# Kernel optimization log

Hardware: AMD Instinct MI355X
Metric: run time of the kernel (lower is better)

The kernel has to match this reference:

```python
import jax, jax.numpy as jnp
import numpy as np

D_MODEL = 512
N_HEADS = 8
D_K = D_MODEL // N_HEADS


def setup_inputs() -> dict:
    key = jax.random.key(0)
    ks = jax.random.split(key, 12)
    B, L = 2, 512
    s = 1.0 / np.sqrt(D_MODEL)
    sk = 1.0 / np.sqrt(D_K)
    return {
        "query": jax.random.normal(ks[0], (B, L, D_MODEL), jnp.float32),
        "key": jax.random.normal(ks[1], (B, L, D_MODEL), jnp.float32),
        "value": jax.random.normal(ks[2], (B, L, D_MODEL), jnp.float32),
        "Wq": jax.random.normal(ks[3], (D_MODEL, D_MODEL), jnp.float32) * s,
        "bq": jnp.zeros((D_MODEL,), jnp.float32),
        "Wk": jax.random.normal(ks[4], (D_MODEL, D_MODEL), jnp.float32) * s,
        "bk": jnp.zeros((D_MODEL,), jnp.float32),
        "Wv": jax.random.normal(ks[5], (D_MODEL, D_MODEL), jnp.float32) * s,
        "bv": jnp.zeros((D_MODEL,), jnp.float32),
        "Wo": jax.random.normal(ks[6], (D_MODEL, D_MODEL), jnp.float32) * s,
        "bo": jnp.zeros((D_MODEL,), jnp.float32),
        "Aq": jax.random.normal(ks[7], (D_K, D_K), jnp.float32) * sk,  # inner W_q (no bias)
        "Ak": jax.random.normal(ks[8], (D_K, D_K), jnp.float32) * sk,  # inner W_k (no bias)
        "av": jax.random.normal(ks[9], (D_K,), jnp.float32) * sk,      # inner v (d_k -> 1)
    }


def _split_heads(x):
    B, L, _ = x.shape
    return x.reshape(B, L, N_HEADS, D_K).transpose(0, 2, 1, 3)  # [B,H,L,dk]


def reference(query, key, value, Wq, bq, Wk, bk, Wv, bv, Wo, bo, Aq, Ak, av):
    # outer projections (torch Linear: x @ W.T + b)
    Q = _split_heads(query @ Wq.T + bq)   # [B,H,Lq,dk]
    K = _split_heads(key @ Wk.T + bk)     # [B,H,Lk,dk]
    V = _split_heads(value @ Wv.T + bv)   # [B,H,Lk,dk]
    # inner additive attention: e_ij = v^T tanh(Aq q_i + Ak k_j)
    qp = Q @ Aq.T                          # [B,H,Lq,dk]
    kp = K @ Ak.T                          # [B,H,Lk,dk]
    energy = jnp.tanh(qp[:, :, :, None, :] + kp[:, :, None, :, :])  # [B,H,Lq,Lk,dk]
    scores = jnp.einsum('bhqkd,d->bhqk', energy, av)
    attn = jax.nn.softmax(scores, axis=-1)  # dropout disabled (eval)
    out = jnp.einsum('bhqk,bhkd->bhqd', attn, V)  # [B,H,Lq,dk]
    B, _, Lq, _ = out.shape
    out = out.transpose(0, 2, 1, 3).reshape(B, Lq, D_MODEL)
    return out @ Wo.T + bo
```

## Files before the change

### kernel.cpp

```cpp
#include <hip/hip_runtime.h>

#define LOG2E 1.4426950408889634f

typedef __bf16 bf16x8 __attribute__((ext_vector_type(8)));
typedef float f32x4 __attribute__((ext_vector_type(4)));
typedef float f32x2 __attribute__((ext_vector_type(2)));
typedef unsigned short u16x8 __attribute__((ext_vector_type(8)));

__device__ __forceinline__ unsigned short bfb(__bf16 b){
  union { __bf16 b; unsigned short u; } z; z.b = b; return z.u;
}


__global__ __launch_bounds__(256) void prep_all(
    const float* __restrict__ Wq, const float* __restrict__ Aq,
    const float* __restrict__ Wk, const float* __restrict__ Ak,
    const float* __restrict__ bq, const float* __restrict__ bk,
    const float* __restrict__ av,
    const float* __restrict__ Wv, const float* __restrict__ Wo,
    const float* __restrict__ Qin, const float* __restrict__ Kin,
    const float* __restrict__ Vin,
    unsigned short* __restrict__ W2qp, unsigned short* __restrict__ W2kp,
    unsigned short* __restrict__ Wvp,  unsigned short* __restrict__ Wop,
    unsigned short* __restrict__ qhi, unsigned short* __restrict__ qlo,
    unsigned short* __restrict__ khi, unsigned short* __restrict__ klo,
    unsigned short* __restrict__ vhi, unsigned short* __restrict__ vlo,
    float* __restrict__ b2q, float* __restrict__ b2k, float* __restrict__ av2g,
    float* __restrict__ zbase){
  if (blockIdx.x >= 513){
    if (blockIdx.y){
      int x = blockIdx.x - 513;
      if (x < 260){
        float* z = zbase + (size_t)(x * 256 + threadIdx.x) * 8;
        f32x4 zz = {0.f, 0.f, 0.f, 0.f};
        *(f32x4*)z = zz;
        *(f32x4*)(z + 4) = zz;
      }
      return;
    }
    int j = blockIdx.x - 513;
    const float* src; unsigned short *dh, *dl;
    if (j < 256){ src = Qin; dh = qhi; dl = qlo; }
    else if (j < 512){ src = Kin; dh = khi; dl = klo; j -= 256; }
    else { src = Vin; dh = vhi; dl = vlo; j -= 512; }
    int base = (j * 256 + threadIdx.x) * 8;
    f32x4 v0 = *(const f32x4*)(src + base);
    f32x4 v1 = *(const f32x4*)(src + base + 4);
    u16x8 hh, ll;
    #pragma unroll
    for (int t = 0; t < 8; t++){
      float f = (t < 4) ? v0[t] : v1[t - 4];
      __bf16 hb = (__bf16)f;
      hh[t] = bfb(hb);
      ll[t] = bfb((__bf16)(f - (float)hb));
    }
    *(u16x8*)(dh + base) = hh;
    *(u16x8*)(dl + base) = ll;
    return;
  }
  if (blockIdx.x >= 256){
    if (blockIdx.x == 512){
      if (blockIdx.y == 0){
        #pragma unroll
        for (int rep = 0; rep < 2; rep++){
          int n = rep * 256 + threadIdx.x;
          int h = n >> 6, e = n & 63;
          float aq = 0.f, ak = 0.f;
          for (int c = 0; c < 64; c++){
            aq += Aq[e*64 + c] * bq[h*64 + c];
            ak += Ak[e*64 + c] * bk[h*64 + c];
          }
          b2q[n] = aq * (2.f * LOG2E);
          b2k[n] = ak * (2.f * LOG2E);
        }
      } else {
        if (threadIdx.x < 64) av2g[threadIdx.x] = -2.f * LOG2E * av[threadIdx.x];
      }
      return;
    }
    const float* src = blockIdx.y ? Wo : Wv;
    unsigned short* dst = blockIdx.y ? Wop : Wvp;
    int base = ((blockIdx.x - 256) * 256 + threadIdx.x) * 4;
    int n = base >> 9, k0 = base & 511;
    float4 v = *(const float4*)(src + base);
    ushort4 h, l;
    float f; __bf16 hb;
    f = v.x; hb = (__bf16)f; h.x = bfb(hb); l.x = bfb((__bf16)(f - (float)hb));
    f = v.y; hb = (__bf16)f; h.y = bfb(hb); l.y = bfb((__bf16)(f - (float)hb));
    f = v.z; hb = (__bf16)f; h.z = bfb(hb); l.z = bfb((__bf16)(f - (float)hb));
    f = v.w; hb = (__bf16)f; h.w = bfb(hb); l.w = bfb((__bf16)(f - (float)hb));
    int nt = n >> 4, ln = n & 15;
    int ks = k0 >> 5, q = (k0 & 31) >> 3, j0 = k0 & 7;
    size_t off = (size_t)((nt*16 + ks) * 2) * 512 + (q*16 + ln) * 8 + j0;
    *(ushort4*)(dst + off)       = h;
    *(ushort4*)(dst + off + 512) = l;
    return;
  }
  const float* W  = blockIdx.y ? Wk : Wq;
  const float* Am = blockIdx.y ? Ak : Aq;
  unsigned short* dst = blockIdx.y ? W2kp : W2qp;
  int idx = blockIdx.x * 256 + threadIdx.x;
  int n = idx >> 7;
  int k0 = (idx & 127) * 4;
  int h = n >> 6, e = n & 63;
  float4 acc = {0.f, 0.f, 0.f, 0.f};
  #pragma unroll 8
  for (int c = 0; c < 64; c++){
    float am = Am[e*64 + c];
    float4 wv = *(const float4*)(W + (size_t)(h*64 + c)*512 + k0);
    acc.x += am * wv.x;
    acc.y += am * wv.y;
    acc.z += am * wv.z;
    acc.w += am * wv.w;
  }
  int nt = n >> 4, ln = n & 15;
  int ks = k0 >> 5, q = (k0 & 31) >> 3, j0 = k0 & 7;
  size_t off = (size_t)((nt*16 + ks) * 2) * 512 + (q*16 + ln) * 8 + j0;
  ushort4 hh, ll;
  float f; __bf16 hb;
  f = acc.x * (2.f * LOG2E); hb = (__bf16)f; hh.x = bfb(hb); ll.x = bfb((__bf16)(f - (float)hb));
  f = acc.y * (2.f * LOG2E); hb = (__bf16)f; hh.y = bfb(hb); ll.y = bfb((__bf16)(f - (float)hb));
  f = acc.z * (2.f * LOG2E); hb = (__bf16)f; hh.z = bfb(hb); ll.z = bfb((__bf16)(f - (float)hb));
  f = acc.w * (2.f * LOG2E); hb = (__bf16)f; hh.w = bfb(hb); ll.w = bfb((__bf16)(f - (float)hb));
  *(ushort4*)(dst + off)       = hh;
  *(ushort4*)(dst + off + 512) = ll;
}

struct GemmBatch {
  const unsigned short* Ahi;
  const unsigned short* Alo;
  const unsigned short* Bp;
  const float* bias;
  float* Cf;
  unsigned short* Chi;
  unsigned short* Clo;
  int transposed;
  int expout;
  int dual;
};
struct GemmArgs { GemmBatch g[3]; };

__global__ __launch_bounds__(256) void gemm_nk(GemmArgs ga){
  GemmBatch gb = ga.g[blockIdx.z];
  __shared__ unsigned short AhiS[32 * 72];
  __shared__ unsigned short AloS[32 * 72];
  const int tid = threadIdx.x, lane = tid & 63, w = tid >> 6;
  const int l15 = lane & 15, quad = lane >> 4;
  const int m0  = blockIdx.x * 32;
  const int nt0 = blockIdx.y * 4;
  const int wr = w >> 1, wc = w & 1;
  f32x4 ac0 = {0.f,0.f,0.f,0.f}, ac1 = ac0;

  const int srow = tid >> 3;
  const int scol = (tid & 7) * 8;
  const unsigned short* srcH = gb.Ahi + (size_t)(m0 + srow) * 512 + scol;
  const unsigned short* srcL = gb.Alo + (size_t)(m0 + srow) * 512 + scol;
  unsigned short* dstH = &AhiS[srow * 72 + scol];
  unsigned short* dstL = &AloS[srow * 72 + scol];
  u16x8 ph = *(const u16x8*)srcH;
  u16x8 pl = *(const u16x8*)srcL;

  const int arow = (wr * 16 + l15) * 72;

  for (int kc = 0; kc < 8; kc++){
    __syncthreads();
    *(u16x8*)dstH = ph;
    *(u16x8*)dstL = pl;
    if (kc < 7){
      ph = *(const u16x8*)(srcH + (kc + 1) * 64);
      pl = *(const u16x8*)(srcL + (kc + 1) * 64);
    }
    __syncthreads();
    #pragma unroll
    for (int s = 0; s < 2; s++){
      int ks = kc * 2 + s;
      bf16x8 ah = *(const bf16x8*)&AhiS[arow + s*32 + quad*8];
      bf16x8 al = *(const bf16x8*)&AloS[arow + s*32 + quad*8];
      #pragma unroll
      for (int t = 0; t < 2; t++){
        int nt = nt0 + wc*2 + t;
        const unsigned short* bp = gb.Bp + (size_t)((nt*16 + ks) * 2) * 512 + lane*8;
        bf16x8 bh = *(const bf16x8*)bp;
        bf16x8 bl = *(const bf16x8*)(bp + 512);
        f32x4& ac = t ? ac1 : ac0;
        ac = __builtin_amdgcn_mfma_f32_16x16x32_bf16(ah, bh, ac, 0, 0, 0);
        ac = __builtin_amdgcn_mfma_f32_16x16x32_bf16(al, bh, ac, 0, 0, 0);
        ac = __builtin_amdgcn_mfma_f32_16x16x32_bf16(ah, bl, ac, 0, 0, 0);
      }
    }
  }

  const int mrow = m0 + wr * 16 + quad * 4;
  #pragma unroll
  for (int t = 0; t < 2; t++){
    f32x4 v = t ? ac1 : ac0;
    int n = nt0*16 + wc*32 + t*16 + l15;
    float bs = gb.bias[n];
    #pragma unroll
    for (int r = 0; r < 4; r++){
      float val = v[r] + bs;
      if (gb.expout) val = __builtin_amdgcn_exp2f(val);
      int m2 = mrow + r;
      if (gb.dual){
        size_t o = (size_t)(((m2 >> 9) * 8 + (n >> 6)) * 64 + (n & 63)) * 512 + (m2 & 511);
        __bf16 hb = (__bf16)val;
        gb.Chi[o] = bfb(hb);
        gb.Clo[o] = bfb((__bf16)(val - (float)hb));
      } else if (gb.transposed){
        gb.Cf[(size_t)(((m2 >> 9) * 8 + (n >> 6)) * 512 + (m2 & 511)) * 64 + (n & 63)] = val;
      } else {
        gb.Cf[(size_t)m2 * 512 + n] = val;
      }
    }
  }
}

__global__ __launch_bounds__(256, 3) void score_pv(
    const float* __restrict__ eqQ, const float* __restrict__ ekp,
    const float* __restrict__ av2g,
    const unsigned short* __restrict__ vthi, const unsigned short* __restrict__ vtlo,
    float* __restrict__ Og, float* __restrict__ deng){
  __shared__ float SHf[12480];
  float* EKt = SHf;
  float* EQs = SHf + 8320;
  float* avS = SHf + 12416;
  unsigned short* Ph = (unsigned short*)SHf;
  unsigned short* Pl = (unsigned short*)SHf + 8704;

  const int tid = threadIdx.x, lane = tid & 63, w = tid >> 6;
  const int l15 = lane & 15, quad = lane >> 4;
  const int bh = blockIdx.z, b = bh >> 3, h = bh & 7;
  const int i0 = blockIdx.y * 64;
  const int j0 = blockIdx.x * 128;

  {
    int r = tid >> 2, c = (tid & 3) * 16;
    const float* s = eqQ + ((size_t)bh * 512 + i0 + r) * 64 + c;
    #pragma unroll
    for (int u = 0; u < 4; u++)
      *(f32x4*)&EQs[r * 64 + c + u * 4] = *(const f32x4*)(s + u * 4);
  }
  if (tid < 64) avS[tid] = av2g[tid];
  {
    int j = tid >> 1, c0 = (tid & 1) * 32;
    const float* s = ekp + ((size_t)(b * 512) + j0 + j) * 512 + h * 64 + c0;
    #pragma unroll
    for (int u = 0; u < 8; u++){
      f32x4 v = *(const f32x4*)(s + u * 4);
      #pragma unroll
      for (int q = 0; q < 4; q++) EKt[(c0 + u * 4 + q) * 130 + j] = v[q];
    }
  }
  __syncthreads();

  f32x2 acc[16];
  #pragma unroll
  for (int ii = 0; ii < 16; ii++) acc[ii] = (f32x2){0.f, 0.f};
  for (int d = 0; d < 64; d += 4){
    f32x2 ek0 = *(const f32x2*)&EKt[(d    ) * 130 + 2 * lane];
    f32x2 ek1 = *(const f32x2*)&EKt[(d + 1) * 130 + 2 * lane];
    f32x2 ek2 = *(const f32x2*)&EKt[(d + 2) * 130 + 2 * lane];
    f32x2 ek3 = *(const f32x2*)&EKt[(d + 3) * 130 + 2 * lane];
    f32x4 a4 = *(const f32x4*)&avS[d];
    #pragma unroll
    for (int ii = 0; ii < 16; ii++){
      f32x4 eq4 = *(const f32x4*)&EQs[(w * 16 + ii) * 64 + d];
      f32x2 A = __builtin_elementwise_fma((f32x2){eq4[0], eq4[0]}, ek0, (f32x2){1.f, 1.f});
      f32x2 B = __builtin_elementwise_fma((f32x2){eq4[1], eq4[1]}, ek1, (f32x2){1.f, 1.f});
      f32x2 t = __builtin_elementwise_fma((f32x2){a4[1], a4[1]}, A, (f32x2){a4[0], a4[0]} * B);
      f32x2 dpr = A * B;
      f32x2 r;
      r.x = __builtin_amdgcn_rcpf(dpr.x);
      r.y = __builtin_amdgcn_rcpf(dpr.y);
      acc[ii] = __builtin_elementwise_fma(t, r, acc[ii]);
      f32x2 C = __builtin_elementwise_fma((f32x2){eq4[2], eq4[2]}, ek2, (f32x2){1.f, 1.f});
      f32x2 D = __builtin_elementwise_fma((f32x2){eq4[3], eq4[3]}, ek3, (f32x2){1.f, 1.f});
      f32x2 t2 = __builtin_elementwise_fma((f32x2){a4[3], a4[3]}, C, (f32x2){a4[2], a4[2]} * D);
      f32x2 dpr2 = C * D;
      f32x2 r2;
      r2.x = __builtin_amdgcn_rcpf(dpr2.x);
      r2.y = __builtin_amdgcn_rcpf(dpr2.y);
      acc[ii] = __builtin_elementwise_fma(t2, r2, acc[ii]);
    }
  }
  #pragma unroll
  for (int ii = 0; ii < 16; ii++){
    acc[ii].x = __builtin_amdgcn_exp2f(acc[ii].x);
    acc[ii].y = __builtin_amdgcn_exp2f(acc[ii].y);
  }
  __syncthreads();
  #pragma unroll
  for (int ii = 0; ii < 16; ii++){
    float s2 = acc[ii].x + acc[ii].y;
    #pragma unroll
    for (int off = 1; off < 64; off <<= 1) s2 += __shfl_xor(s2, off, 64);
    if (lane == 0) atomicAdd(&deng[bh * 512 + i0 + w * 16 + ii], s2);
    __bf16 h0 = (__bf16)acc[ii].x, h1 = (__bf16)acc[ii].y;
    ushort2 hi = { bfb(h0), bfb(h1) };
    ushort2 lo = { bfb((__bf16)(acc[ii].x - (float)h0)), bfb((__bf16)(acc[ii].y - (float)h1)) };
    *(ushort2*)&Ph[(w * 16 + ii) * 136 + 2 * lane] = hi;
    *(ushort2*)&Pl[(w * 16 + ii) * 136 + 2 * lane] = lo;
  }
  __syncthreads();

  f32x4 o0 = {0.f,0.f,0.f,0.f}, o1 = o0, o2 = o0, o3 = o0;
  const size_t vbase = ((size_t)bh * 64) * 512 + j0;
  #pragma unroll
  for (int ks = 0; ks < 4; ks++){
    bf16x8 pa = *(const bf16x8*)&Ph[(w * 16 + l15) * 136 + ks * 32 + quad * 8];
    bf16x8 pb = *(const bf16x8*)&Pl[(w * 16 + l15) * 136 + ks * 32 + quad * 8];
    #pragma unroll
    for (int nt = 0; nt < 4; nt++){
      size_t vo = vbase + (size_t)(nt * 16 + l15) * 512 + ks * 32 + quad * 8;
      bf16x8 vh = *(const bf16x8*)(vthi + vo);
      bf16x8 vl = *(const bf16x8*)(vtlo + vo);
      f32x4& o = nt == 0 ? o0 : nt == 1 ? o1 : nt == 2 ? o2 : o3;
      o = __builtin_amdgcn_mfma_f32_16x16x32_bf16(pa, vh, o, 0, 0, 0);
      o = __builtin_amdgcn_mfma_f32_16x16x32_bf16(pb, vh, o, 0, 0, 0);
      o = __builtin_amdgcn_mfma_f32_16x16x32_bf16(pa, vl, o, 0, 0, 0);
    }
  }
  #pragma unroll
  for (int nt = 0; nt < 4; nt++){
    f32x4 o = nt == 0 ? o0 : nt == 1 ? o1 : nt == 2 ? o2 : o3;
    int d = nt * 16 + l15;
    #pragma unroll
    for (int r = 0; r < 4; r++){
      int i = i0 + w * 16 + quad * 4 + r;
      atomicAdd(&Og[((size_t)bh * 512 + i) * 64 + d], o[r]);
    }
  }
}

__global__ __launch_bounds__(256) void finish_oh(
    const float* __restrict__ Og, const float* __restrict__ deng,
    unsigned short* __restrict__ Ohhi, unsigned short* __restrict__ Ohlo){
  int t = blockIdx.x * 256 + threadIdx.x;
  int bh = t >> 12;
  int i  = (t >> 3) & 511;
  int d0 = (t & 7) * 8;
  float rv = 1.0f / deng[bh * 512 + i];
  const float* src = Og + ((size_t)bh * 512 + i) * 64 + d0;
  f32x4 v0 = *(const f32x4*)src;
  f32x4 v1 = *(const f32x4*)(src + 4);
  u16x8 hh, ll;
  #pragma unroll
  for (int u = 0; u < 8; u++){
    float f = ((u < 4) ? v0[u] : v1[u - 4]) * rv;
    __bf16 hb = (__bf16)f;
    hh[u] = bfb(hb);
    ll[u] = bfb((__bf16)(f - (float)hb));
  }
  size_t o = ((size_t)(bh >> 3) * 512 + i) * 512 + (bh & 7) * 64 + d0;
  *(u16x8*)(Ohhi + o) = hh;
  *(u16x8*)(Ohlo + o) = ll;
}

extern "C" void kernel_launch(void* const* d_in, const int* in_sizes, int n_in,
                              void* d_out, int out_size, void* d_ws, size_t ws_size,
                              hipStream_t stream){
  const float* q_in = (const float*)d_in[0];
  const float* k_in = (const float*)d_in[1];
  const float* v_in = (const float*)d_in[2];
  const float* Wq_  = (const float*)d_in[3];
  const float* bq_  = (const float*)d_in[4];
  const float* Wk_  = (const float*)d_in[5];
  const float* bk_  = (const float*)d_in[6];
  const float* Wv_  = (const float*)d_in[7];
  const float* bv_  = (const float*)d_in[8];
  const float* Wo_  = (const float*)d_in[9];
  const float* bo_  = (const float*)d_in[10];
  const float* Aq_  = (const float*)d_in[11];
  const float* Ak_  = (const float*)d_in[12];
  const float* av_  = (const float*)d_in[13];

  char* ws = (char*)d_ws;
  unsigned short* W2qp = (unsigned short*)(ws + 0);
  unsigned short* W2kp = (unsigned short*)(ws + 1048576);
  unsigned short* Ohhi = (unsigned short*)(ws + 0);
  unsigned short* Ohlo = (unsigned short*)(ws + 1048576);
  unsigned short* Wvp  = (unsigned short*)(ws + 2097152);
  unsigned short* Wop  = (unsigned short*)(ws + 3145728);
  float* b2q  = (float*)(ws + 4194304);
  float* b2k  = (float*)(ws + 4196352);
  float* av2g = (float*)(ws + 4198400);
  float* eqQ  = (float*)(ws + 4198656);
  float* ekp  = (float*)(ws + 6295808);
  unsigned short* vthi = (unsigned short*)(ws + 8392960);
  unsigned short* vtlo = (unsigned short*)(ws + 9441536);
  unsigned short* qhi = (unsigned short*)(ws + 10490112);
  unsigned short* qlo = (unsigned short*)(ws + 11538688);
  unsigned short* khi = (unsigned short*)(ws + 12587264);
  unsigned short* klo = (unsigned short*)(ws + 13635840);
  unsigned short* vhi = (unsigned short*)(ws + 14684416);
  unsigned short* vlo = (unsigned short*)(ws + 15732992);
  float* deng = (float*)(ws + 16781568);
  float* Og   = (float*)(ws + 16814336);

  prep_all<<<dim3(1281, 2, 1), 256, 0, stream>>>(Wq_, Aq_, Wk_, Ak_, bq_, bk_, av_,
                                                 Wv_, Wo_, q_in, k_in, v_in,
                                                 W2qp, W2kp, Wvp, Wop,
                                                 qhi, qlo, khi, klo, vhi, vlo,
                                                 b2q, b2k, av2g, deng);

  GemmArgs ga;
  ga.g[0] = { qhi, qlo, W2qp, b2q, eqQ, 0, 0, 1, 1, 0 };
  ga.g[1] = { khi, klo, W2kp, b2k, ekp, 0, 0, 0, 1, 0 };
  ga.g[2] = { vhi, vlo, Wvp,  bv_, 0, vthi, vtlo, 0, 0, 1 };
  gemm_nk<<<dim3(32, 8, 3), 256, 0, stream>>>(ga);

  score_pv<<<dim3(4, 8, 16), 256, 0, stream>>>(eqQ, ekp, av2g, vthi, vtlo, Og, deng);

  finish_oh<<<dim3(256, 1, 1), 256, 0, stream>>>(Og, deng, Ohhi, Ohlo);

  GemmArgs go;
  go.g[0] = { Ohhi, Ohlo, Wop, bo_, (float*)d_out, 0, 0, 0, 0, 0 };
  go.g[1] = go.g[0];
  go.g[2] = go.g[0];
  gemm_nk<<<dim3(32, 8, 1), 256, 0, stream>>>(go);
}
```

Baseline: 163.6 us.

## Split score kernel key range across twice the waves and stage dual GEMM output

The score_pv kernel now runs 512 threads per block. Each wave pair covers the same 16 query rows but a different 64-key half, so each lane handles one key instead of two. The two halves' P·V partial results are summed in shared memory before one set of atomics, which halves the global atomic traffic to the output buffer. In the projection GEMM, the transposed bf16 hi/lo output for V is first staged through shared memory so it can be written with 16-byte coalesced stores instead of scattered 2-byte stores. The cost is a tighter per-thread register budget from the new launch bounds and an extra barrier and LDS round trip.

```diff
diff --git a/kernel.cpp b/kernel.cpp
--- a/kernel.cpp
+++ b/kernel.cpp
@@ -142,8 +142,8 @@
 
 __global__ __launch_bounds__(256) void gemm_nk(GemmArgs ga){
   GemmBatch gb = ga.g[blockIdx.z];
-  __shared__ unsigned short AhiS[32 * 72];
-  __shared__ unsigned short AloS[32 * 72];
+  __shared__ unsigned short AhiS[64 * 40];
+  __shared__ unsigned short AloS[64 * 40];
   const int tid = threadIdx.x, lane = tid & 63, w = tid >> 6;
   const int l15 = lane & 15, quad = lane >> 4;
   const int m0  = blockIdx.x * 32;
@@ -190,6 +190,32 @@
     }
   }
 
+  if (gb.dual){
+    __syncthreads();
+    #pragma unroll
+    for (int t = 0; t < 2; t++){
+      f32x4 v = t ? ac1 : ac0;
+      int nl = wc*32 + t*16 + l15;
+      float bs = gb.bias[nt0*16 + nl];
+      #pragma unroll
+      for (int r = 0; r < 4; r++){
+        float val = v[r] + bs;
+        int ml = wr*16 + quad*4 + r;
+        __bf16 hb = (__bf16)val;
+        AhiS[nl*40 + ml] = bfb(hb);
+        AloS[nl*40 + ml] = bfb((__bf16)(val - (float)hb));
+      }
+    }
+    __syncthreads();
+    int nl = tid >> 2, mq = (tid & 3) * 8;
+    int hh2 = (nt0 * 16) >> 6;
+    int b2 = m0 >> 9;
+    size_t o = (size_t)((b2*8 + hh2)*64 + ((nt0*16 + nl) & 63)) * 512 + (m0 & 511) + mq;
+    *(u16x8*)(gb.Chi + o) = *(const u16x8*)&AhiS[nl*40 + mq];
+    *(u16x8*)(gb.Clo + o) = *(const u16x8*)&AloS[nl*40 + mq];
+    return;
+  }
+
   const int mrow = m0 + wr * 16 + quad * 4;
   #pragma unroll
   for (int t = 0; t < 2; t++){
@@ -201,12 +227,7 @@
       float val = v[r] + bs;
       if (gb.expout) val = __builtin_amdgcn_exp2f(val);
       int m2 = mrow + r;
-      if (gb.dual){
-        size_t o = (size_t)(((m2 >> 9) * 8 + (n >> 6)) * 64 + (n & 63)) * 512 + (m2 & 511);
-        __bf16 hb = (__bf16)val;
-        gb.Chi[o] = bfb(hb);
-        gb.Clo[o] = bfb((__bf16)(val - (float)hb));
-      } else if (gb.transposed){
+      if (gb.transposed){
         gb.Cf[(size_t)(((m2 >> 9) * 8 + (n >> 6)) * 512 + (m2 & 511)) * 64 + (n & 63)] = val;
       } else {
         gb.Cf[(size_t)m2 * 512 + n] = val;
@@ -215,33 +236,27 @@
   }
 }
 
-__global__ __launch_bounds__(256, 3) void score_pv(
+__global__ __launch_bounds__(512, 4) void score_pv(
     const float* __restrict__ eqQ, const float* __restrict__ ekp,
     const float* __restrict__ av2g,
     const unsigned short* __restrict__ vthi, const unsigned short* __restrict__ vtlo,
     float* __restrict__ Og, float* __restrict__ deng){
-  __shared__ float SHf[12480];
+  __shared__ float SHf[12864];
   float* EKt = SHf;
   float* EQs = SHf + 8320;
-  float* avS = SHf + 12416;
+  float* avS = SHf + 12800;
   unsigned short* Ph = (unsigned short*)SHf;
   unsigned short* Pl = (unsigned short*)SHf + 8704;
+  float* cmb = SHf + 8704;
 
   const int tid = threadIdx.x, lane = tid & 63, w = tid >> 6;
   const int l15 = lane & 15, quad = lane >> 4;
   const int bh = blockIdx.z, b = bh >> 3, h = bh & 7;
   const int i0 = blockIdx.y * 64;
   const int j0 = blockIdx.x * 128;
-
-  {
-    int r = tid >> 2, c = (tid & 3) * 16;
-    const float* s = eqQ + ((size_t)bh * 512 + i0 + r) * 64 + c;
-    #pragma unroll
-    for (int u = 0; u < 4; u++)
-      *(f32x4*)&EQs[r * 64 + c + u * 4] = *(const f32x4*)(s + u * 4);
-  }
-  if (tid < 64) avS[tid] = av2g[tid];
-  {
+  const int wi = w >> 1, jh = w & 1;
+
+  if (tid < 256){
     int j = tid >> 1, c0 = (tid & 1) * 32;
     const float* s = ekp + ((size_t)(b * 512) + j0 + j) * 512 + h * 64 + c0;
     #pragma unroll
@@ -250,65 +265,63 @@
       #pragma unroll
       for (int q = 0; q < 4; q++) EKt[(c0 + u * 4 + q) * 130 + j] = v[q];
     }
+  } else {
+    int t2 = tid - 256;
+    int r = t2 >> 2, c = (t2 & 3) * 16;
+    const float* s = eqQ + ((size_t)bh * 512 + i0 + r) * 64 + c;
+    #pragma unroll
+    for (int u = 0; u < 4; u++)
+      *(f32x4*)&EQs[r * 64 + c + u * 4] = *(const f32x4*)(s + u * 4);
+    if (t2 < 64) avS[t2] = av2g[t2];
   }
   __syncthreads();
 
-  f32x2 acc[16];
-  #pragma unroll
-  for (int ii = 0; ii < 16; ii++) acc[ii] = (f32x2){0.f, 0.f};
+  float acc[16];
+  #pragma unroll
+  for (int ii = 0; ii < 16; ii++) acc[ii] = 0.f;
+  const int jl = jh * 64 + lane;
   for (int d = 0; d < 64; d += 4){
-    f32x2 ek0 = *(const f32x2*)&EKt[(d    ) * 130 + 2 * lane];
-    f32x2 ek1 = *(const f32x2*)&EKt[(d + 1) * 130 + 2 * lane];
-    f32x2 ek2 = *(const f32x2*)&EKt[(d + 2) * 130 + 2 * lane];
-    f32x2 ek3 = *(const f32x2*)&EKt[(d + 3) * 130 + 2 * lane];
+    float ek0 = EKt[(d    ) * 130 + jl];
+    float ek1 = EKt[(d + 1) * 130 + jl];
+    float ek2 = EKt[(d + 2) * 130 + jl];
+    float ek3 = EKt[(d + 3) * 130 + jl];
     f32x4 a4 = *(const f32x4*)&avS[d];
     #pragma unroll
     for (int ii = 0; ii < 16; ii++){
-      f32x4 eq4 = *(const f32x4*)&EQs[(w * 16 + ii) * 64 + d];
-      f32x2 A = __builtin_elementwise_fma((f32x2){eq4[0], eq4[0]}, ek0, (f32x2){1.f, 1.f});
-      f32x2 B = __builtin_elementwise_fma((f32x2){eq4[1], eq4[1]}, ek1, (f32x2){1.f, 1.f});
-      f32x2 t = __builtin_elementwise_fma((f32x2){a4[1], a4[1]}, A, (f32x2){a4[0], a4[0]} * B);
-      f32x2 dpr = A * B;
-      f32x2 r;
-      r.x = __builtin_amdgcn_rcpf(dpr.x);
-      r.y = __builtin_amdgcn_rcpf(dpr.y);
-      acc[ii] = __builtin_elementwise_fma(t, r, acc[ii]);
-      f32x2 C = __builtin_elementwise_fma((f32x2){eq4[2], eq4[2]}, ek2, (f32x2){1.f, 1.f});
-      f32x2 D = __builtin_elementwise_fma((f32x2){eq4[3], eq4[3]}, ek3, (f32x2){1.f, 1.f});
-      f32x2 t2 = __builtin_elementwise_fma((f32x2){a4[3], a4[3]}, C, (f32x2){a4[2], a4[2]} * D);
-      f32x2 dpr2 = C * D;
-      f32x2 r2;
-      r2.x = __builtin_amdgcn_rcpf(dpr2.x);
-      r2.y = __builtin_amdgcn_rcpf(dpr2.y);
-      acc[ii] = __builtin_elementwise_fma(t2, r2, acc[ii]);
-    }
-  }
+      f32x4 eq4 = *(const f32x4*)&EQs[(wi * 16 + ii) * 64 + d];
+      float A = __builtin_fmaf(eq4[0], ek0, 1.f);
+      float B = __builtin_fmaf(eq4[1], ek1, 1.f);
+      float t = __builtin_fmaf(a4[1], A, a4[0] * B);
+      acc[ii] = __builtin_fmaf(t, __builtin_amdgcn_rcpf(A * B), acc[ii]);
+      float C = __builtin_fmaf(eq4[2], ek2, 1.f);
+      float D = __builtin_fmaf(eq4[3], ek3, 1.f);
+      float t2 = __builtin_fmaf(a4[3], C, a4[2] * D);
+      acc[ii] = __builtin_fmaf(t2, __builtin_amdgcn_rcpf(C * D), acc[ii]);
+    }
+  }
+  #pragma unroll
+  for (int ii = 0; ii < 16; ii++) acc[ii] = __builtin_amdgcn_exp2f(acc[ii]);
+  __syncthreads();
+
   #pragma unroll
   for (int ii = 0; ii < 16; ii++){
-    acc[ii].x = __builtin_amdgcn_exp2f(acc[ii].x);
-    acc[ii].y = __builtin_amdgcn_exp2f(acc[ii].y);
-  }
-  __syncthreads();
-  #pragma unroll
-  for (int ii = 0; ii < 16; ii++){
-    float s2 = acc[ii].x + acc[ii].y;
+    float s2 = acc[ii];
     #pragma unroll
     for (int off = 1; off < 64; off <<= 1) s2 += __shfl_xor(s2, off, 64);
-    if (lane == 0) atomicAdd(&deng[bh * 512 + i0 + w * 16 + ii], s2);
-    __bf16 h0 = (__bf16)acc[ii].x, h1 = (__bf16)acc[ii].y;
-    ushort2 hi = { bfb(h0), bfb(h1) };
-    ushort2 lo = { bfb((__bf16)(acc[ii].x - (float)h0)), bfb((__bf16)(acc[ii].y - (float)h1)) };
-    *(ushort2*)&Ph[(w * 16 + ii) * 136 + 2 * lane] = hi;
-    *(ushort2*)&Pl[(w * 16 + ii) * 136 + 2 * lane] = lo;
-  }
-  __syncthreads();
+    if (lane == 0) atomicAdd(&deng[bh * 512 + i0 + wi * 16 + ii], s2);
+    float e = acc[ii];
+    __bf16 hb = (__bf16)e;
+    Ph[(wi * 16 + ii) * 136 + jl] = bfb(hb);
+    Pl[(wi * 16 + ii) * 136 + jl] = bfb((__bf16)(e - (float)hb));
+  }
 
   f32x4 o0 = {0.f,0.f,0.f,0.f}, o1 = o0, o2 = o0, o3 = o0;
-  const size_t vbase = ((size_t)bh * 64) * 512 + j0;
-  #pragma unroll
-  for (int ks = 0; ks < 4; ks++){
-    bf16x8 pa = *(const bf16x8*)&Ph[(w * 16 + l15) * 136 + ks * 32 + quad * 8];
-    bf16x8 pb = *(const bf16x8*)&Pl[(w * 16 + l15) * 136 + ks * 32 + quad * 8];
+  const size_t vbase = ((size_t)bh * 64) * 512 + j0 + jh * 64;
+  #pragma unroll
+  for (int ks = 0; ks < 2; ks++){
+    int k0 = jh * 64 + ks * 32 + quad * 8;
+    bf16x8 pa = *(const bf16x8*)&Ph[(wi * 16 + l15) * 136 + k0];
+    bf16x8 pb = *(const bf16x8*)&Pl[(wi * 16 + l15) * 136 + k0];
     #pragma unroll
     for (int nt = 0; nt < 4; nt++){
       size_t vo = vbase + (size_t)(nt * 16 + l15) * 512 + ks * 32 + quad * 8;
@@ -320,14 +333,27 @@
       o = __builtin_amdgcn_mfma_f32_16x16x32_bf16(pa, vl, o, 0, 0, 0);
     }
   }
-  #pragma unroll
-  for (int nt = 0; nt < 4; nt++){
-    f32x4 o = nt == 0 ? o0 : nt == 1 ? o1 : nt == 2 ? o2 : o3;
-    int d = nt * 16 + l15;
-    #pragma unroll
-    for (int r = 0; r < 4; r++){
-      int i = i0 + w * 16 + quad * 4 + r;
-      atomicAdd(&Og[((size_t)bh * 512 + i) * 64 + d], o[r]);
+  if (jh == 1){
+    #pragma unroll
+    for (int nt = 0; nt < 4; nt++){
+      f32x4 o = nt == 0 ? o0 : nt == 1 ? o1 : nt == 2 ? o2 : o3;
+      #pragma unroll
+      for (int r = 0; r < 4; r++)
+        cmb[(wi * 16 + quad * 4 + r) * 64 + nt * 16 + l15] = o[r];
+    }
+  }
+  __syncthreads();
+  if (jh == 0){
+    #pragma unroll
+    for (int nt = 0; nt < 4; nt++){
+      f32x4 o = nt == 0 ? o0 : nt == 1 ? o1 : nt == 2 ? o2 : o3;
+      int d = nt * 16 + l15;
+      #pragma unroll
+      for (int r = 0; r < 4; r++){
+        int il = wi * 16 + quad * 4 + r;
+        float cv = o[r] + cmb[il * 64 + d];
+        atomicAdd(&Og[((size_t)bh * 512 + i0 + il) * 64 + d], cv);
+      }
     }
   }
 }
@@ -409,7 +435,7 @@
   ga.g[2] = { vhi, vlo, Wvp,  bv_, 0, vthi, vtlo, 0, 0, 1 };
   gemm_nk<<<dim3(32, 8, 3), 256, 0, stream>>>(ga);
 
-  score_pv<<<dim3(4, 8, 16), 256, 0, stream>>>(eqQ, ekp, av2g, vthi, vtlo, Og, deng);
+  score_pv<<<dim3(4, 8, 16), 512, 0, stream>>>(eqQ, ekp, av2g, vthi, vtlo, Og, deng);
 
   finish_oh<<<dim3(256, 1, 1), 256, 0, stream>>>(Og, deng, Ohhi, Ohlo);
 
```

Result: faster. 157.4 us (-3.8%).
